# Kernel tuning notes

Measured on AMD Instinct MI355X. Metric: run time of the kernel, lower is better.

The kernel has to match this reference:

```python
import jax, jax.numpy as jnp
import numpy as np

N, D = 1024, 256  # number of matrices (power of 2), matrix dim
EPS = 0.002       # near-identity noise scale to keep 1024-long product stable


def setup_inputs() -> dict:
    key = jax.random.key(0)
    k1, k2 = jax.random.split(key)
    x = jax.random.normal(k1, (1, D), dtype=jnp.float32)
    m = jnp.eye(D, dtype=jnp.float32)[None] + EPS * jax.random.normal(
        k2, (N, D, D), dtype=jnp.float32)
    return {"x": x, "m": m}


def reference(x, m):
    # The torch module performs a Blelloch up-sweep (pairwise bmm) building
    # per-level products, then a down-sweep producing the exclusive prefix
    # applications of x: res[k] = x @ (m_0 @ ... @ m_{k-1}) for k = 0..N.
    # lax.associative_scan with matmul is the idiomatic log-depth tree scan
    # computing the same math: P[k] = m_0 @ ... @ m_k (inclusive, in order).
    P = jax.lax.associative_scan(jnp.matmul, m)      # [N, D, D]
    applied = jnp.matmul(x, P)[:, 0, :]              # [N, D]: x @ P[k]
    # res[0] = x (empty prefix), res[1..N] = x @ P[0..N-1]
    res = jnp.concatenate([x, applied], axis=0)      # [N+1, D]
    return res
```

## Files before the change

### kernel.cpp

```cpp
#include <hip/hip_runtime.h>
#include <hip/hip_bf16.h>


#define D 256
#define DD 65536

typedef __attribute__((ext_vector_type(8))) short short8;
typedef __attribute__((ext_vector_type(4))) float f4;

__device__ __forceinline__ float bf2f(unsigned short u) {
  return __uint_as_float(((unsigned)u) << 16);
}
__device__ __forceinline__ unsigned short f2bf(float f) {
  __hip_bfloat16 h = __float2bfloat16(f);
  unsigned short u;
  __builtin_memcpy(&u, &h, 2);
  return u;
}
__device__ __forceinline__ unsigned f2bf2(float lo, float hi) {
  __hip_bfloat162 h = __float22bfloat162_rn(make_float2(lo, hi));
  unsigned u;
  __builtin_memcpy(&u, &h, 4);
  return u;
}
#define LSWZ(i15, lq) (((((i15) & 15)) + ((lq) << 4)) ^ (lq))

__global__ __launch_bounds__(256, 4) void gemm_mfma(
    const float* __restrict__ aF, const unsigned short* __restrict__ aBf,
    long aMul, long aOff,
    const float* __restrict__ bF, const unsigned short* __restrict__ bBf,
    long bMul, long bOff,
    unsigned short* __restrict__ out)
{
  __shared__ __attribute__((aligned(16))) unsigned short Bs[16384];

  const int  bx  = blockIdx.x;
  const int  nmb = ((int)gridDim.x) >> 4;
  const int  xcd = bx & 7, q = bx >> 3;
  const long mat = (long)(xcd * (nmb >> 3)) + (q >> 4);
  const int  tile = q & 15;
  const int  m0 = (tile >> 2) << 6, n0 = (tile & 3) << 6;
  const long aBase = (mat * aMul + aOff) * (long)DD;
  const long bBase = (mat * bMul + bOff) * (long)DD;
  const int t = threadIdx.x;
  const int w = t >> 6, l = t & 63, lm = l & 15, lq4 = l >> 4;
  const int lswz = l ^ lq4;

  const int R = m0 + (w << 4) + lm;
  short8 areg[8];
  if (aF) {
    const float* ap = aF + aBase + (long)R * D + (lq4 << 3);
#pragma unroll
    for (int kt = 0; kt < 8; ++kt) {
      float4 v0 = *(const float4*)(ap + (kt << 5));
      float4 v1 = *(const float4*)(ap + (kt << 5) + 4);
      if ((R >> 3) == (kt << 2) + lq4) {
        const int j = R & 7;
        if      (j == 0) v0.x -= 1.f;
        else if (j == 1) v0.y -= 1.f;
        else if (j == 2) v0.z -= 1.f;
        else if (j == 3) v0.w -= 1.f;
        else if (j == 4) v1.x -= 1.f;
        else if (j == 5) v1.y -= 1.f;
        else if (j == 6) v1.z -= 1.f;
        else             v1.w -= 1.f;
      }
      union { short8 v8; unsigned u[4]; } ou;
      ou.u[0] = f2bf2(v0.x, v0.y);
      ou.u[1] = f2bf2(v0.z, v0.w);
      ou.u[2] = f2bf2(v1.x, v1.y);
      ou.u[3] = f2bf2(v1.z, v1.w);
      areg[kt] = ou.v8;
    }
  } else {
    const unsigned short* ap = aBf + aBase + (long)R * D + (lq4 << 3);
#pragma unroll
    for (int kt = 0; kt < 8; ++kt)
      areg[kt] = *(const short8*)(ap + (kt << 5));
  }

  {
    const int n4 = (t & 15) << 2;
    const int kb0 = (t >> 4) << 3;
    const int gn = n0 + n4;
#pragma unroll
    for (int kp = 0; kp < 2; ++kp) {
      const int k8 = kb0 + (kp << 7);
      const int lq = (k8 >> 3) & 3, kt = k8 >> 5;
      if (bF) {
        unsigned tmpu[4][4];
        const int rel = gn - k8;
#pragma unroll
        for (int h = 0; h < 2; ++h) {
          float4 va[2], vb[2];
#pragma unroll
          for (int p2 = 0; p2 < 2; ++p2) {
            va[p2] = *(const float4*)(bF + bBase + (long)(k8 + 4 * h + 2 * p2) * D + gn);
            vb[p2] = *(const float4*)(bF + bBase + (long)(k8 + 4 * h + 2 * p2 + 1) * D + gn);
          }
          if (rel == 4 * h) {
            va[0].x -= 1.f; vb[0].y -= 1.f; va[1].z -= 1.f; vb[1].w -= 1.f;
          }
          tmpu[0][2 * h + 0] = f2bf2(va[0].x, vb[0].x);
          tmpu[0][2 * h + 1] = f2bf2(va[1].x, vb[1].x);
          tmpu[1][2 * h + 0] = f2bf2(va[0].y, vb[0].y);
          tmpu[1][2 * h + 1] = f2bf2(va[1].y, vb[1].y);
          tmpu[2][2 * h + 0] = f2bf2(va[0].z, vb[0].z);
          tmpu[2][2 * h + 1] = f2bf2(va[1].z, vb[1].z);
          tmpu[3][2 * h + 0] = f2bf2(va[0].w, vb[0].w);
          tmpu[3][2 * h + 1] = f2bf2(va[1].w, vb[1].w);
        }
#pragma unroll
        for (int jj = 0; jj < 4; ++jj) {
          const int n = n4 + jj;
          const int slot = (((n >> 4) << 3) + kt) * 64 + LSWZ(n, lq);
          uint4 st = { tmpu[jj][0], tmpu[jj][1], tmpu[jj][2], tmpu[jj][3] };
          *(uint4*)&Bs[slot << 3] = st;
        }
      } else {
        __attribute__((aligned(16))) unsigned short tmp[4][8];
#pragma unroll
        for (int kk = 0; kk < 8; ++kk) {
          const ushort4 v = *(const ushort4*)(bBf + bBase + (long)(k8 + kk) * D + gn);
          tmp[0][kk] = v.x; tmp[1][kk] = v.y; tmp[2][kk] = v.z; tmp[3][kk] = v.w;
        }
#pragma unroll
        for (int jj = 0; jj < 4; ++jj) {
          const int n = n4 + jj;
          const int slot = (((n >> 4) << 3) + kt) * 64 + LSWZ(n, lq);
          *(uint4*)&Bs[slot << 3] = *(const uint4*)&tmp[jj][0];
        }
      }
    }
  }
  __syncthreads();

  f4 acc[4] = {{0.f,0.f,0.f,0.f},{0.f,0.f,0.f,0.f},
               {0.f,0.f,0.f,0.f},{0.f,0.f,0.f,0.f}};
#pragma unroll
  for (int kt = 0; kt < 8; ++kt) {
#pragma unroll
    for (int f = 0; f < 4; ++f) {
      const short8 b = *(const short8*)&Bs[((((f << 3) + kt) << 6) + lswz) << 3];
      acc[f] = __builtin_amdgcn_mfma_f32_16x16x32_bf16(areg[kt], b, acc[f], 0, 0, 0);
    }
  }

#pragma unroll
  for (int f = 0; f < 4; ++f) {
    const int gj_l = (f << 4) + lm;
    const int gj   = n0 + gj_l;
#pragma unroll
    for (int r = 0; r < 4; ++r) {
      const int gi_l = (w << 4) + (lq4 << 2) + r;
      const int giG  = m0 + gi_l;
      float da;
      if (aF)
        da = aF[aBase + (long)giG * D + gj] - ((giG == gj) ? 1.f : 0.f);
      else
        da = bf2f(aBf[aBase + (long)giG * D + gj]);
      const int lqB  = (giG >> 3) & 3;
      const int slotB = (((gj_l >> 4) << 3) + (giG >> 5)) * 64 + LSWZ(gj_l, lqB);
      const float db = bf2f(Bs[(slotB << 3) + (giG & 7)]);
      acc[f][r] += da + db;
    }
  }
  __syncthreads();

  unsigned short* Cs = Bs;
#pragma unroll
  for (int f = 0; f < 4; ++f)
#pragma unroll
    for (int r = 0; r < 4; ++r)
      Cs[((w << 4) + (lq4 << 2) + r) * 66 + (f << 4) + lm] = f2bf(acc[f][r]);
  __syncthreads();
  {
    const int row = t >> 2, c0g = (t & 3) << 4;
    const unsigned int* Cw = (const unsigned int*)Cs;
    const int wb = row * 33 + ((t & 3) << 3);
    unsigned int wbuf[8];
#pragma unroll
    for (int i = 0; i < 8; ++i) wbuf[i] = Cw[wb + i];
    unsigned short* og = out + mat * (long)DD + (long)(m0 + row) * D + n0 + c0g;
    uint4 o0 = { wbuf[0], wbuf[1], wbuf[2], wbuf[3] };
    uint4 o1 = { wbuf[4], wbuf[5], wbuf[6], wbuf[7] };
    *(uint4*)og = o0;
    *((uint4*)og + 1) = o1;
  }
}

__device__ __forceinline__ void apply_bf16(const unsigned short* __restrict__ Mb,
                                           float* v, float (*ps)[D],
                                           int t, int col, int kq) {
  const unsigned short* M = Mb + (long)(kq * 64) * D + col;
  float acc = 0.f;
#pragma unroll 8
  for (int i = 0; i < 64; ++i)
    acc += v[kq * 64 + i] * bf2f(M[(long)i * D]);
  ps[kq][col] = acc;
  __syncthreads();
  if (t < D) v[t] += ps[0][t] + ps[1][t] + ps[2][t] + ps[3][t];
  __syncthreads();
}

__global__ __launch_bounds__(1024) void tail_fused(
    const float* __restrict__ x,
    const unsigned short* __restrict__ sp128, const unsigned short* __restrict__ sp64,
    const unsigned short* __restrict__ sp32,  const unsigned short* __restrict__ sp16,
    const unsigned short* __restrict__ sp8,   const unsigned short* __restrict__ sp4,
    const float* __restrict__ m, float* __restrict__ out)
{
  __shared__ float v[D];
  __shared__ float ps[4][D];
  const int c = blockIdx.x, t = threadIdx.x, col = t & 255, kq = t >> 8;
  if (t < D) v[t] = x[t];
  __syncthreads();
  const int L = c << 2;

  int pos = 0;
#pragma unroll 1
  while (pos + 128 <= L) { apply_bf16(sp128 + (long)(pos >> 7) * DD, v, ps, t, col, kq); pos += 128; }
  if (pos + 64 <= L) { apply_bf16(sp64 + (long)(pos >> 6) * DD, v, ps, t, col, kq); pos += 64; }
  if (pos + 32 <= L) { apply_bf16(sp32 + (long)(pos >> 5) * DD, v, ps, t, col, kq); pos += 32; }
  if (pos + 16 <= L) { apply_bf16(sp16 + (long)(pos >> 4) * DD, v, ps, t, col, kq); pos += 16; }
  if (pos + 8 <= L)  { apply_bf16(sp8  + (long)(pos >> 3) * DD, v, ps, t, col, kq); pos += 8; }
  if (pos + 4 <= L)  { apply_bf16(sp4  + (long)(pos >> 2) * DD, v, ps, t, col, kq); pos += 4; }

  if (t < D) out[(long)L * D + t] = v[t];
  const int steps = (c == 255) ? 4 : 3;
#pragma unroll 1
  for (int s = 0; s < steps; ++s) {
    const float* M = m + (long)(L + s) * DD + (long)(kq * 64) * D + col;
    float acc = 0.f;
#pragma unroll 8
    for (int i = 0; i < 64; ++i)
      acc += v[kq * 64 + i] * M[(long)i * D];
    ps[kq][col] = acc;
    __syncthreads();
    if (t < D) {
      const float s2 = ps[0][t] + ps[1][t] + ps[2][t] + ps[3][t];
      v[t] = s2;
      out[(long)(L + s + 1) * D + t] = s2;
    }
    __syncthreads();
  }
}

__global__ __launch_bounds__(256) void fallback_seq(
    const float* __restrict__ x, const float* __restrict__ m,
    float* __restrict__ out)
{
  __shared__ float v[D];
  const int t = threadIdx.x;
  v[t] = x[t];
  __syncthreads();
  for (int k = 0; k < 1024; ++k) {
    out[(long)k * D + t] = v[t];
    const float* M = m + (long)k * DD;
    float acc = 0.f;
    for (int i = 0; i < D; ++i) acc += v[i] * M[(long)i * D + t];
    __syncthreads();
    v[t] = acc;
    __syncthreads();
  }
  out[(long)1024 * D + t] = v[t];
}

extern "C" void kernel_launch(void* const* d_in, const int* in_sizes, int n_in,
                              void* d_out, int out_size, void* d_ws, size_t ws_size,
                              hipStream_t stream) {
  const float* x = (const float*)d_in[0];
  const float* m = (const float*)d_in[1];
  float* out = (float*)d_out;

  char* w8 = (char*)d_ws;
  const size_t MB = 1048576;
  const dim3 blk(256), vblk(1024);

  if (ws_size >= 127 * MB) {
    unsigned short* T2   = (unsigned short*)(w8);
    unsigned short* Qb   = (unsigned short*)(w8 + 64 * MB);
    unsigned short* Q2   = (unsigned short*)(w8 + 96 * MB);
    unsigned short* Q4   = (unsigned short*)(w8 + 112 * MB);
    unsigned short* Rm   = (unsigned short*)(w8 + 120 * MB);
    unsigned short* S64  = (unsigned short*)(w8 + 124 * MB);
    unsigned short* S128 = (unsigned short*)(w8 + 126 * MB);
    gemm_mfma<<<dim3(8192), blk, 0, stream>>>(m, nullptr, 2, 0, m, nullptr, 2, 1, T2);
    gemm_mfma<<<dim3(4096), blk, 0, stream>>>(nullptr, T2, 2, 0, nullptr, T2, 2, 1, Qb);
    gemm_mfma<<<dim3(2048), blk, 0, stream>>>(nullptr, Qb, 2, 0, nullptr, Qb, 2, 1, Q2);
    gemm_mfma<<<dim3(1024), blk, 0, stream>>>(nullptr, Q2, 2, 0, nullptr, Q2, 2, 1, Q4);
    gemm_mfma<<<dim3(512),  blk, 0, stream>>>(nullptr, Q4, 2, 0, nullptr, Q4, 2, 1, Rm);
    gemm_mfma<<<dim3(256),  blk, 0, stream>>>(nullptr, Rm, 2, 0, nullptr, Rm, 2, 1, S64);
    gemm_mfma<<<dim3(128),  blk, 0, stream>>>(nullptr, S64, 2, 0, nullptr, S64, 2, 1, S128);
    tail_fused<<<dim3(256), vblk, 0, stream>>>(x, S128, S64, Rm, Q4, Q2, Qb, m, out);
  } else if (ws_size >= 67108864) {
    unsigned short* buf0 = (unsigned short*)(w8);
    unsigned short* Qb   = (unsigned short*)(w8 + 33554432);
    unsigned short* Q2   = (unsigned short*)(w8);
    unsigned short* Q4   = (unsigned short*)(w8 + 16777216);
    unsigned short* Rm   = (unsigned short*)(w8 + 25165824);
    unsigned short* S64  = (unsigned short*)(w8 + 29360128);
    unsigned short* S128 = (unsigned short*)(w8 + 31457280);
    gemm_mfma<<<dim3(4096), blk, 0, stream>>>(m, nullptr, 2, 0, m, nullptr, 2, 1, buf0);
    gemm_mfma<<<dim3(2048), blk, 0, stream>>>(nullptr, buf0, 2, 0, nullptr, buf0, 2, 1, Qb);
    gemm_mfma<<<dim3(4096), blk, 0, stream>>>(m + 512L * DD, nullptr, 2, 0,
                                              m + 512L * DD, nullptr, 2, 1, buf0);
    gemm_mfma<<<dim3(2048), blk, 0, stream>>>(nullptr, buf0, 2, 0, nullptr, buf0, 2, 1,
                                              Qb + 128L * DD);
    gemm_mfma<<<dim3(2048), blk, 0, stream>>>(nullptr, Qb, 2, 0, nullptr, Qb, 2, 1, Q2);
    gemm_mfma<<<dim3(1024), blk, 0, stream>>>(nullptr, Q2, 2, 0, nullptr, Q2, 2, 1, Q4);
    gemm_mfma<<<dim3(512),  blk, 0, stream>>>(nullptr, Q4, 2, 0, nullptr, Q4, 2, 1, Rm);
    gemm_mfma<<<dim3(256),  blk, 0, stream>>>(nullptr, Rm, 2, 0, nullptr, Rm, 2, 1, S64);
    gemm_mfma<<<dim3(128),  blk, 0, stream>>>(nullptr, S64, 2, 0, nullptr, S64, 2, 1, S128);
    tail_fused<<<dim3(256), vblk, 0, stream>>>(x, S128, S64, Rm, Q4, Q2, Qb, m, out);
  } else {
    fallback_seq<<<dim3(1), blk, 0, stream>>>(x, m, out);
  }
}
```

Measured before the change: 569.1 us.

## Switch pairwise GEMM to 128x128 tiles with K-looped LDS staging

Reworks the pairwise matrix-product kernel so each block computes a 128x128 output tile instead of 64x64, staging both A and B through LDS in 64-wide K steps. Each wave now computes a 4x4 grid of MFMA fragments, which raises operand reuse and cuts the number of blocks by four. The epilogue writes bf16 directly to global memory instead of going through an LDS transpose, and the residual terms are reloaded from global. The risks are fewer blocks for the small late levels (as few as 32), uncoalesced 2-byte stores, and more accumulator registers with the occupancy hint dropped.

```diff
diff --git a/kernel.cpp b/kernel.cpp
--- a/kernel.cpp
+++ b/kernel.cpp
@@ -24,79 +24,88 @@
   return u;
 }
 #define LSWZ(i15, lq) (((((i15) & 15)) + ((lq) << 4)) ^ (lq))
-
-__global__ __launch_bounds__(256, 4) void gemm_mfma(
+#define PSLOT(r, k8) (((((r) >> 4) << 1) + ((k8) >> 5)) * 64 + LSWZ((r), ((k8) >> 3) & 3))
+
+__global__ __launch_bounds__(256) void gemm_mfma(
     const float* __restrict__ aF, const unsigned short* __restrict__ aBf,
     long aMul, long aOff,
     const float* __restrict__ bF, const unsigned short* __restrict__ bBf,
     long bMul, long bOff,
     unsigned short* __restrict__ out)
 {
-  __shared__ __attribute__((aligned(16))) unsigned short Bs[16384];
+  __shared__ __attribute__((aligned(16))) unsigned short As[8192];
+  __shared__ __attribute__((aligned(16))) unsigned short Bs[8192];
 
   const int  bx  = blockIdx.x;
-  const int  nmb = ((int)gridDim.x) >> 4;
+  const int  nmb = ((int)gridDim.x) >> 2;
   const int  xcd = bx & 7, q = bx >> 3;
-  const long mat = (long)(xcd * (nmb >> 3)) + (q >> 4);
-  const int  tile = q & 15;
-  const int  m0 = (tile >> 2) << 6, n0 = (tile & 3) << 6;
+  const long mat = (long)(xcd * (nmb >> 3)) + (q >> 2);
+  const int  tile = q & 3;
+  const int  m0 = (tile >> 1) << 7, n0 = (tile & 1) << 7;
   const long aBase = (mat * aMul + aOff) * (long)DD;
   const long bBase = (mat * bMul + bOff) * (long)DD;
   const int t = threadIdx.x;
   const int w = t >> 6, l = t & 63, lm = l & 15, lq4 = l >> 4;
   const int lswz = l ^ lq4;
-
-  const int R = m0 + (w << 4) + lm;
-  short8 areg[8];
-  if (aF) {
-    const float* ap = aF + aBase + (long)R * D + (lq4 << 3);
-#pragma unroll
-    for (int kt = 0; kt < 8; ++kt) {
-      float4 v0 = *(const float4*)(ap + (kt << 5));
-      float4 v1 = *(const float4*)(ap + (kt << 5) + 4);
-      if ((R >> 3) == (kt << 2) + lq4) {
-        const int j = R & 7;
-        if      (j == 0) v0.x -= 1.f;
-        else if (j == 1) v0.y -= 1.f;
-        else if (j == 2) v0.z -= 1.f;
-        else if (j == 3) v0.w -= 1.f;
-        else if (j == 4) v1.x -= 1.f;
-        else if (j == 5) v1.y -= 1.f;
-        else if (j == 6) v1.z -= 1.f;
-        else             v1.w -= 1.f;
-      }
-      union { short8 v8; unsigned u[4]; } ou;
-      ou.u[0] = f2bf2(v0.x, v0.y);
-      ou.u[1] = f2bf2(v0.z, v0.w);
-      ou.u[2] = f2bf2(v1.x, v1.y);
-      ou.u[3] = f2bf2(v1.z, v1.w);
-      areg[kt] = ou.v8;
-    }
-  } else {
-    const unsigned short* ap = aBf + aBase + (long)R * D + (lq4 << 3);
-#pragma unroll
-    for (int kt = 0; kt < 8; ++kt)
-      areg[kt] = *(const short8*)(ap + (kt << 5));
-  }
-
-  {
-    const int n4 = (t & 15) << 2;
-    const int kb0 = (t >> 4) << 3;
-    const int gn = n0 + n4;
-#pragma unroll
-    for (int kp = 0; kp < 2; ++kp) {
-      const int k8 = kb0 + (kp << 7);
-      const int lq = (k8 >> 3) & 3, kt = k8 >> 5;
+  const int wr = w >> 1, wc = w & 1;
+
+  f4 acc[4][4];
+#pragma unroll
+  for (int i = 0; i < 4; ++i)
+#pragma unroll
+    for (int f = 0; f < 4; ++f)
+      acc[i][f] = (f4){0.f, 0.f, 0.f, 0.f};
+
+  for (int step = 0; step < 4; ++step) {
+    const int kb = step << 6;
+    if (aF) {
+#pragma unroll
+      for (int p = 0; p < 4; ++p) {
+        const int cell = t + (p << 8);
+        const int row = cell >> 3, k8 = (cell & 7) << 3;
+        const int rg = m0 + row, kg = kb + k8;
+        const float* ap = aF + aBase + (long)rg * D + kg;
+        float4 v0 = *(const float4*)ap;
+        float4 v1 = *(const float4*)(ap + 4);
+        const int dj = rg - kg;
+        if (((unsigned)dj) < 8u) {
+          if      (dj == 0) v0.x -= 1.f;
+          else if (dj == 1) v0.y -= 1.f;
+          else if (dj == 2) v0.z -= 1.f;
+          else if (dj == 3) v0.w -= 1.f;
+          else if (dj == 4) v1.x -= 1.f;
+          else if (dj == 5) v1.y -= 1.f;
+          else if (dj == 6) v1.z -= 1.f;
+          else              v1.w -= 1.f;
+        }
+        union { short8 v8; unsigned u[4]; } ou;
+        ou.u[0] = f2bf2(v0.x, v0.y); ou.u[1] = f2bf2(v0.z, v0.w);
+        ou.u[2] = f2bf2(v1.x, v1.y); ou.u[3] = f2bf2(v1.z, v1.w);
+        *(short8*)&As[PSLOT(row, k8) << 3] = ou.v8;
+      }
+    } else {
+#pragma unroll
+      for (int p = 0; p < 4; ++p) {
+        const int cell = t + (p << 8);
+        const int row = cell >> 3, k8 = (cell & 7) << 3;
+        const short8 v = *(const short8*)(aBf + aBase + (long)(m0 + row) * D + kb + k8);
+        *(short8*)&As[PSLOT(row, k8) << 3] = v;
+      }
+    }
+    {
+      const int n4 = (t & 31) << 2;
+      const int k8 = (t >> 5) << 3;
+      const int gn = n0 + n4, kg = kb + k8;
       if (bF) {
         unsigned tmpu[4][4];
-        const int rel = gn - k8;
+        const int rel = gn - kg;
 #pragma unroll
         for (int h = 0; h < 2; ++h) {
           float4 va[2], vb[2];
 #pragma unroll
           for (int p2 = 0; p2 < 2; ++p2) {
-            va[p2] = *(const float4*)(bF + bBase + (long)(k8 + 4 * h + 2 * p2) * D + gn);
-            vb[p2] = *(const float4*)(bF + bBase + (long)(k8 + 4 * h + 2 * p2 + 1) * D + gn);
+            va[p2] = *(const float4*)(bF + bBase + (long)(kg + 4 * h + 2 * p2) * D + gn);
+            vb[p2] = *(const float4*)(bF + bBase + (long)(kg + 4 * h + 2 * p2 + 1) * D + gn);
           }
           if (rel == 4 * h) {
             va[0].x -= 1.f; vb[0].y -= 1.f; va[1].z -= 1.f; vb[1].w -= 1.f;
@@ -113,79 +122,59 @@
 #pragma unroll
         for (int jj = 0; jj < 4; ++jj) {
           const int n = n4 + jj;
-          const int slot = (((n >> 4) << 3) + kt) * 64 + LSWZ(n, lq);
           uint4 st = { tmpu[jj][0], tmpu[jj][1], tmpu[jj][2], tmpu[jj][3] };
-          *(uint4*)&Bs[slot << 3] = st;
+          *(uint4*)&Bs[PSLOT(n, k8) << 3] = st;
         }
       } else {
         __attribute__((aligned(16))) unsigned short tmp[4][8];
 #pragma unroll
         for (int kk = 0; kk < 8; ++kk) {
-          const ushort4 v = *(const ushort4*)(bBf + bBase + (long)(k8 + kk) * D + gn);
+          const ushort4 v = *(const ushort4*)(bBf + bBase + (long)(kg + kk) * D + gn);
           tmp[0][kk] = v.x; tmp[1][kk] = v.y; tmp[2][kk] = v.z; tmp[3][kk] = v.w;
         }
 #pragma unroll
         for (int jj = 0; jj < 4; ++jj) {
           const int n = n4 + jj;
-          const int slot = (((n >> 4) << 3) + kt) * 64 + LSWZ(n, lq);
-          *(uint4*)&Bs[slot << 3] = *(const uint4*)&tmp[jj][0];
-        }
-      }
-    }
-  }
-  __syncthreads();
-
-  f4 acc[4] = {{0.f,0.f,0.f,0.f},{0.f,0.f,0.f,0.f},
-               {0.f,0.f,0.f,0.f},{0.f,0.f,0.f,0.f}};
-#pragma unroll
-  for (int kt = 0; kt < 8; ++kt) {
-#pragma unroll
-    for (int f = 0; f < 4; ++f) {
-      const short8 b = *(const short8*)&Bs[((((f << 3) + kt) << 6) + lswz) << 3];
-      acc[f] = __builtin_amdgcn_mfma_f32_16x16x32_bf16(areg[kt], b, acc[f], 0, 0, 0);
-    }
-  }
-
-#pragma unroll
-  for (int f = 0; f < 4; ++f) {
-    const int gj_l = (f << 4) + lm;
-    const int gj   = n0 + gj_l;
+          *(uint4*)&Bs[PSLOT(n, k8) << 3] = *(const uint4*)&tmp[jj][0];
+        }
+      }
+    }
+    __syncthreads();
+#pragma unroll
+    for (int kt = 0; kt < 2; ++kt) {
+      short8 a_[4];
+#pragma unroll
+      for (int i = 0; i < 4; ++i)
+        a_[i] = *(const short8*)&As[(((((wr << 2) + i) << 1) + kt) * 64 + lswz) << 3];
+#pragma unroll
+      for (int f = 0; f < 4; ++f) {
+        const short8 b = *(const short8*)&Bs[(((((wc << 2) + f) << 1) + kt) * 64 + lswz) << 3];
+#pragma unroll
+        for (int i = 0; i < 4; ++i)
+          acc[i][f] = __builtin_amdgcn_mfma_f32_16x16x32_bf16(a_[i], b, acc[i][f], 0, 0, 0);
+      }
+    }
+    __syncthreads();
+  }
+
+#pragma unroll
+  for (int i = 0; i < 4; ++i) {
 #pragma unroll
     for (int r = 0; r < 4; ++r) {
-      const int gi_l = (w << 4) + (lq4 << 2) + r;
-      const int giG  = m0 + gi_l;
-      float da;
-      if (aF)
-        da = aF[aBase + (long)giG * D + gj] - ((giG == gj) ? 1.f : 0.f);
-      else
-        da = bf2f(aBf[aBase + (long)giG * D + gj]);
-      const int lqB  = (giG >> 3) & 3;
-      const int slotB = (((gj_l >> 4) << 3) + (giG >> 5)) * 64 + LSWZ(gj_l, lqB);
-      const float db = bf2f(Bs[(slotB << 3) + (giG & 7)]);
-      acc[f][r] += da + db;
-    }
-  }
-  __syncthreads();
-
-  unsigned short* Cs = Bs;
-#pragma unroll
-  for (int f = 0; f < 4; ++f)
-#pragma unroll
-    for (int r = 0; r < 4; ++r)
-      Cs[((w << 4) + (lq4 << 2) + r) * 66 + (f << 4) + lm] = f2bf(acc[f][r]);
-  __syncthreads();
-  {
-    const int row = t >> 2, c0g = (t & 3) << 4;
-    const unsigned int* Cw = (const unsigned int*)Cs;
-    const int wb = row * 33 + ((t & 3) << 3);
-    unsigned int wbuf[8];
-#pragma unroll
-    for (int i = 0; i < 8; ++i) wbuf[i] = Cw[wb + i];
-    unsigned short* og = out + mat * (long)DD + (long)(m0 + row) * D + n0 + c0g;
-    uint4 o0 = { wbuf[0], wbuf[1], wbuf[2], wbuf[3] };
-    uint4 o1 = { wbuf[4], wbuf[5], wbuf[6], wbuf[7] };
-    *(uint4*)og = o0;
-    *((uint4*)og + 1) = o1;
+      const int rowg = m0 + (wr << 6) + (i << 4) + (lq4 << 2) + r;
+      const long rA = aBase + (long)rowg * D;
+      const long rB = bBase + (long)rowg * D;
+      const long rO = mat * (long)DD + (long)rowg * D;
+#pragma unroll
+      for (int f = 0; f < 4; ++f) {
+        const int colg = n0 + (wc << 6) + (f << 4) + lm;
+        const float da = aF ? (aF[rA + colg] - ((rowg == colg) ? 1.f : 0.f))
+                            : bf2f(aBf[rA + colg]);
+        const float db = bF ? (bF[rB + colg] - ((rowg == colg) ? 1.f : 0.f))
+                            : bf2f(bBf[rB + colg]);
+        out[rO + colg] = f2bf(acc[i][f][r] + da + db);
+      }
+    }
   }
 }
 
@@ -285,13 +274,13 @@
     unsigned short* Rm   = (unsigned short*)(w8 + 120 * MB);
     unsigned short* S64  = (unsigned short*)(w8 + 124 * MB);
     unsigned short* S128 = (unsigned short*)(w8 + 126 * MB);
-    gemm_mfma<<<dim3(8192), blk, 0, stream>>>(m, nullptr, 2, 0, m, nullptr, 2, 1, T2);
-    gemm_mfma<<<dim3(4096), blk, 0, stream>>>(nullptr, T2, 2, 0, nullptr, T2, 2, 1, Qb);
-    gemm_mfma<<<dim3(2048), blk, 0, stream>>>(nullptr, Qb, 2, 0, nullptr, Qb, 2, 1, Q2);
-    gemm_mfma<<<dim3(1024), blk, 0, stream>>>(nullptr, Q2, 2, 0, nullptr, Q2, 2, 1, Q4);
-    gemm_mfma<<<dim3(512),  blk, 0, stream>>>(nullptr, Q4, 2, 0, nullptr, Q4, 2, 1, Rm);
-    gemm_mfma<<<dim3(256),  blk, 0, stream>>>(nullptr, Rm, 2, 0, nullptr, Rm, 2, 1, S64);
-    gemm_mfma<<<dim3(128),  blk, 0, stream>>>(nullptr, S64, 2, 0, nullptr, S64, 2, 1, S128);
+    gemm_mfma<<<dim3(2048), blk, 0, stream>>>(m, nullptr, 2, 0, m, nullptr, 2, 1, T2);
+    gemm_mfma<<<dim3(1024), blk, 0, stream>>>(nullptr, T2, 2, 0, nullptr, T2, 2, 1, Qb);
+    gemm_mfma<<<dim3(512),  blk, 0, stream>>>(nullptr, Qb, 2, 0, nullptr, Qb, 2, 1, Q2);
+    gemm_mfma<<<dim3(256),  blk, 0, stream>>>(nullptr, Q2, 2, 0, nullptr, Q2, 2, 1, Q4);
+    gemm_mfma<<<dim3(128),  blk, 0, stream>>>(nullptr, Q4, 2, 0, nullptr, Q4, 2, 1, Rm);
+    gemm_mfma<<<dim3(64),   blk, 0, stream>>>(nullptr, Rm, 2, 0, nullptr, Rm, 2, 1, S64);
+    gemm_mfma<<<dim3(32),   blk, 0, stream>>>(nullptr, S64, 2, 0, nullptr, S64, 2, 1, S128);
     tail_fused<<<dim3(256), vblk, 0, stream>>>(x, S128, S64, Rm, Q4, Q2, Qb, m, out);
   } else if (ws_size >= 67108864) {
     unsigned short* buf0 = (unsigned short*)(w8);
@@ -301,17 +290,17 @@
     unsigned short* Rm   = (unsigned short*)(w8 + 25165824);
     unsigned short* S64  = (unsigned short*)(w8 + 29360128);
     unsigned short* S128 = (unsigned short*)(w8 + 31457280);
-    gemm_mfma<<<dim3(4096), blk, 0, stream>>>(m, nullptr, 2, 0, m, nullptr, 2, 1, buf0);
-    gemm_mfma<<<dim3(2048), blk, 0, stream>>>(nullptr, buf0, 2, 0, nullptr, buf0, 2, 1, Qb);
-    gemm_mfma<<<dim3(4096), blk, 0, stream>>>(m + 512L * DD, nullptr, 2, 0,
+    gemm_mfma<<<dim3(1024), blk, 0, stream>>>(m, nullptr, 2, 0, m, nullptr, 2, 1, buf0);
+    gemm_mfma<<<dim3(512),  blk, 0, stream>>>(nullptr, buf0, 2, 0, nullptr, buf0, 2, 1, Qb);
+    gemm_mfma<<<dim3(1024), blk, 0, stream>>>(m + 512L * DD, nullptr, 2, 0,
                                               m + 512L * DD, nullptr, 2, 1, buf0);
-    gemm_mfma<<<dim3(2048), blk, 0, stream>>>(nullptr, buf0, 2, 0, nullptr, buf0, 2, 1,
+    gemm_mfma<<<dim3(512),  blk, 0, stream>>>(nullptr, buf0, 2, 0, nullptr, buf0, 2, 1,
                                               Qb + 128L * DD);
-    gemm_mfma<<<dim3(2048), blk, 0, stream>>>(nullptr, Qb, 2, 0, nullptr, Qb, 2, 1, Q2);
-    gemm_mfma<<<dim3(1024), blk, 0, stream>>>(nullptr, Q2, 2, 0, nullptr, Q2, 2, 1, Q4);
-    gemm_mfma<<<dim3(512),  blk, 0, stream>>>(nullptr, Q4, 2, 0, nullptr, Q4, 2, 1, Rm);
-    gemm_mfma<<<dim3(256),  blk, 0, stream>>>(nullptr, Rm, 2, 0, nullptr, Rm, 2, 1, S64);
-    gemm_mfma<<<dim3(128),  blk, 0, stream>>>(nullptr, S64, 2, 0, nullptr, S64, 2, 1, S128);
+    gemm_mfma<<<dim3(512),  blk, 0, stream>>>(nullptr, Qb, 2, 0, nullptr, Qb, 2, 1, Q2);
+    gemm_mfma<<<dim3(256),  blk, 0, stream>>>(nullptr, Q2, 2, 0, nullptr, Q2, 2, 1, Q4);
+    gemm_mfma<<<dim3(128),  blk, 0, stream>>>(nullptr, Q4, 2, 0, nullptr, Q4, 2, 1, Rm);
+    gemm_mfma<<<dim3(64),   blk, 0, stream>>>(nullptr, Rm, 2, 0, nullptr, Rm, 2, 1, S64);
+    gemm_mfma<<<dim3(32),   blk, 0, stream>>>(nullptr, S64, 2, 0, nullptr, S64, 2, 1, S128);
     tail_fused<<<dim3(256), vblk, 0, stream>>>(x, S128, S64, Rm, Q4, Q2, Qb, m, out);
   } else {
     fallback_seq<<<dim3(1), blk, 0, stream>>>(x, m, out);
```

Result: slower. 754.0 us (+32.5%).

## Fuse up-sweep GEMM levels into one cooperative kernel and vectorize tail matvec

Applied to the files above, without the earlier changes.

Replaces seven separate per-level GEMM launches with one persistent cooperative kernel of 1024 blocks. It loops over tree levels with grid-wide syncs between them, which removes launch gaps and tail effects of the shrinking late levels. The tail matvec now gives each thread four columns with 16-row chunks and vector loads, reduced across 16 partial rows in shared memory. Risks: the cooperative launch needs all 1024 blocks co-resident, and grid.sync costs extra; the code falls back to the old launches if the cooperative launch fails.

```diff
diff --git a/kernel.cpp b/kernel.cpp
--- a/kernel.cpp
+++ b/kernel.cpp
@@ -1,5 +1,8 @@
 #include <hip/hip_runtime.h>
 #include <hip/hip_bf16.h>
+#include <hip/hip_cooperative_groups.h>
+
+namespace cg = cooperative_groups;
 
 
 #define D 256
@@ -25,18 +28,17 @@
 }
 #define LSWZ(i15, lq) (((((i15) & 15)) + ((lq) << 4)) ^ (lq))
 
-__global__ __launch_bounds__(256, 4) void gemm_mfma(
+__device__ __forceinline__ void do_tile(
     const float* __restrict__ aF, const unsigned short* __restrict__ aBf,
     long aMul, long aOff,
     const float* __restrict__ bF, const unsigned short* __restrict__ bBf,
     long bMul, long bOff,
-    unsigned short* __restrict__ out)
+    unsigned short* __restrict__ out, int job, int njobs)
 {
   __shared__ __attribute__((aligned(16))) unsigned short Bs[16384];
 
-  const int  bx  = blockIdx.x;
-  const int  nmb = ((int)gridDim.x) >> 4;
-  const int  xcd = bx & 7, q = bx >> 3;
+  const int  nmb = njobs >> 4;
+  const int  xcd = job & 7, q = job >> 3;
   const long mat = (long)(xcd * (nmb >> 3)) + (q >> 4);
   const int  tile = q & 15;
   const int  m0 = (tile >> 2) << 6, n0 = (tile & 3) << 6;
@@ -187,19 +189,60 @@
     *(uint4*)og = o0;
     *((uint4*)og + 1) = o1;
   }
+  __syncthreads();
+}
+
+__global__ __launch_bounds__(256, 4) void gemm_mfma(
+    const float* __restrict__ aF, const unsigned short* __restrict__ aBf,
+    long aMul, long aOff,
+    const float* __restrict__ bF, const unsigned short* __restrict__ bBf,
+    long bMul, long bOff,
+    unsigned short* __restrict__ out)
+{
+  do_tile(aF, aBf, aMul, aOff, bF, bBf, bMul, bOff, out, blockIdx.x, gridDim.x);
+}
+
+__global__ __launch_bounds__(256, 4) void tree_coop(
+    const float* __restrict__ m,
+    unsigned short* __restrict__ T2,  unsigned short* __restrict__ Qb,
+    unsigned short* __restrict__ Q2,  unsigned short* __restrict__ Q4,
+    unsigned short* __restrict__ Rm,  unsigned short* __restrict__ S64,
+    unsigned short* __restrict__ S128)
+{
+  cg::grid_group grid = cg::this_grid();
+  unsigned short* outs[7] = {T2, Qb, Q2, Q4, Rm, S64, S128};
+#pragma unroll 1
+  for (int lev = 0; lev < 7; ++lev) {
+    const int njobs = 8192 >> lev;
+    const float* aF = (lev == 0) ? m : nullptr;
+    const unsigned short* aB = (lev == 0) ? nullptr : outs[lev - 1];
+#pragma unroll 1
+    for (int job = blockIdx.x; job < njobs; job += gridDim.x)
+      do_tile(aF, aB, 2, 0, aF, aB, 2, 1, outs[lev], job, njobs);
+    grid.sync();
+  }
 }
 
 __device__ __forceinline__ void apply_bf16(const unsigned short* __restrict__ Mb,
                                            float* v, float (*ps)[D],
-                                           int t, int col, int kq) {
-  const unsigned short* M = Mb + (long)(kq * 64) * D + col;
-  float acc = 0.f;
-#pragma unroll 8
-  for (int i = 0; i < 64; ++i)
-    acc += v[kq * 64 + i] * bf2f(M[(long)i * D]);
-  ps[kq][col] = acc;
-  __syncthreads();
-  if (t < D) v[t] += ps[0][t] + ps[1][t] + ps[2][t] + ps[3][t];
+                                           int t, int col4, int q) {
+  const unsigned short* Mp = Mb + (long)(q * 16) * D + col4;
+  float a0 = 0.f, a1 = 0.f, a2 = 0.f, a3 = 0.f;
+#pragma unroll
+  for (int i = 0; i < 16; ++i) {
+    const ushort4 u = *(const ushort4*)(Mp + (long)i * D);
+    const float vi = v[q * 16 + i];
+    a0 += vi * bf2f(u.x); a1 += vi * bf2f(u.y);
+    a2 += vi * bf2f(u.z); a3 += vi * bf2f(u.w);
+  }
+  *(float4*)&ps[q][col4] = make_float4(a0, a1, a2, a3);
+  __syncthreads();
+  if (t < D) {
+    float s = 0.f;
+#pragma unroll
+    for (int j = 0; j < 16; ++j) s += ps[j][t];
+    v[t] += s;
+  }
   __syncthreads();
 }
 
@@ -211,34 +254,40 @@
     const float* __restrict__ m, float* __restrict__ out)
 {
   __shared__ float v[D];
-  __shared__ float ps[4][D];
-  const int c = blockIdx.x, t = threadIdx.x, col = t & 255, kq = t >> 8;
+  __shared__ float ps[16][D];
+  const int c = blockIdx.x, t = threadIdx.x;
+  const int col4 = (t & 63) << 2, q = t >> 6;
   if (t < D) v[t] = x[t];
   __syncthreads();
   const int L = c << 2;
 
   int pos = 0;
 #pragma unroll 1
-  while (pos + 128 <= L) { apply_bf16(sp128 + (long)(pos >> 7) * DD, v, ps, t, col, kq); pos += 128; }
-  if (pos + 64 <= L) { apply_bf16(sp64 + (long)(pos >> 6) * DD, v, ps, t, col, kq); pos += 64; }
-  if (pos + 32 <= L) { apply_bf16(sp32 + (long)(pos >> 5) * DD, v, ps, t, col, kq); pos += 32; }
-  if (pos + 16 <= L) { apply_bf16(sp16 + (long)(pos >> 4) * DD, v, ps, t, col, kq); pos += 16; }
-  if (pos + 8 <= L)  { apply_bf16(sp8  + (long)(pos >> 3) * DD, v, ps, t, col, kq); pos += 8; }
-  if (pos + 4 <= L)  { apply_bf16(sp4  + (long)(pos >> 2) * DD, v, ps, t, col, kq); pos += 4; }
+  while (pos + 128 <= L) { apply_bf16(sp128 + (long)(pos >> 7) * DD, v, ps, t, col4, q); pos += 128; }
+  if (pos + 64 <= L) { apply_bf16(sp64 + (long)(pos >> 6) * DD, v, ps, t, col4, q); pos += 64; }
+  if (pos + 32 <= L) { apply_bf16(sp32 + (long)(pos >> 5) * DD, v, ps, t, col4, q); pos += 32; }
+  if (pos + 16 <= L) { apply_bf16(sp16 + (long)(pos >> 4) * DD, v, ps, t, col4, q); pos += 16; }
+  if (pos + 8 <= L)  { apply_bf16(sp8  + (long)(pos >> 3) * DD, v, ps, t, col4, q); pos += 8; }
+  if (pos + 4 <= L)  { apply_bf16(sp4  + (long)(pos >> 2) * DD, v, ps, t, col4, q); pos += 4; }
 
   if (t < D) out[(long)L * D + t] = v[t];
   const int steps = (c == 255) ? 4 : 3;
 #pragma unroll 1
   for (int s = 0; s < steps; ++s) {
-    const float* M = m + (long)(L + s) * DD + (long)(kq * 64) * D + col;
-    float acc = 0.f;
-#pragma unroll 8
-    for (int i = 0; i < 64; ++i)
-      acc += v[kq * 64 + i] * M[(long)i * D];
-    ps[kq][col] = acc;
+    const float* Mp = m + (long)(L + s) * DD + (long)(q * 16) * D + col4;
+    float a0 = 0.f, a1 = 0.f, a2 = 0.f, a3 = 0.f;
+#pragma unroll
+    for (int i = 0; i < 16; ++i) {
+      const float4 u = *(const float4*)(Mp + (long)i * D);
+      const float vi = v[q * 16 + i];
+      a0 += vi * u.x; a1 += vi * u.y; a2 += vi * u.z; a3 += vi * u.w;
+    }
+    *(float4*)&ps[q][col4] = make_float4(a0, a1, a2, a3);
     __syncthreads();
     if (t < D) {
-      const float s2 = ps[0][t] + ps[1][t] + ps[2][t] + ps[3][t];
+      float s2 = 0.f;
+#pragma unroll
+      for (int j = 0; j < 16; ++j) s2 += ps[j][t];
       v[t] = s2;
       out[(long)(L + s + 1) * D + t] = s2;
     }
@@ -285,13 +334,20 @@
     unsigned short* Rm   = (unsigned short*)(w8 + 120 * MB);
     unsigned short* S64  = (unsigned short*)(w8 + 124 * MB);
     unsigned short* S128 = (unsigned short*)(w8 + 126 * MB);
-    gemm_mfma<<<dim3(8192), blk, 0, stream>>>(m, nullptr, 2, 0, m, nullptr, 2, 1, T2);
-    gemm_mfma<<<dim3(4096), blk, 0, stream>>>(nullptr, T2, 2, 0, nullptr, T2, 2, 1, Qb);
-    gemm_mfma<<<dim3(2048), blk, 0, stream>>>(nullptr, Qb, 2, 0, nullptr, Qb, 2, 1, Q2);
-    gemm_mfma<<<dim3(1024), blk, 0, stream>>>(nullptr, Q2, 2, 0, nullptr, Q2, 2, 1, Q4);
-    gemm_mfma<<<dim3(512),  blk, 0, stream>>>(nullptr, Q4, 2, 0, nullptr, Q4, 2, 1, Rm);
-    gemm_mfma<<<dim3(256),  blk, 0, stream>>>(nullptr, Rm, 2, 0, nullptr, Rm, 2, 1, S64);
-    gemm_mfma<<<dim3(128),  blk, 0, stream>>>(nullptr, S64, 2, 0, nullptr, S64, 2, 1, S128);
+    const float* mm = m;
+    void* args[] = { (void*)&mm, (void*)&T2, (void*)&Qb, (void*)&Q2,
+                     (void*)&Q4, (void*)&Rm, (void*)&S64, (void*)&S128 };
+    hipError_t e = hipLaunchCooperativeKernel((const void*)tree_coop,
+                                              dim3(1024), blk, args, 0, stream);
+    if (e != hipSuccess) {
+      gemm_mfma<<<dim3(8192), blk, 0, stream>>>(m, nullptr, 2, 0, m, nullptr, 2, 1, T2);
+      gemm_mfma<<<dim3(4096), blk, 0, stream>>>(nullptr, T2, 2, 0, nullptr, T2, 2, 1, Qb);
+      gemm_mfma<<<dim3(2048), blk, 0, stream>>>(nullptr, Qb, 2, 0, nullptr, Qb, 2, 1, Q2);
+      gemm_mfma<<<dim3(1024), blk, 0, stream>>>(nullptr, Q2, 2, 0, nullptr, Q2, 2, 1, Q4);
+      gemm_mfma<<<dim3(512),  blk, 0, stream>>>(nullptr, Q4, 2, 0, nullptr, Q4, 2, 1, Rm);
+      gemm_mfma<<<dim3(256),  blk, 0, stream>>>(nullptr, Rm, 2, 0, nullptr, Rm, 2, 1, S64);
+      gemm_mfma<<<dim3(128),  blk, 0, stream>>>(nullptr, S64, 2, 0, nullptr, S64, 2, 1, S128);
+    }
     tail_fused<<<dim3(256), vblk, 0, stream>>>(x, S128, S64, Rm, Q4, Q2, Qb, m, out);
   } else if (ws_size >= 67108864) {
     unsigned short* buf0 = (unsigned short*)(w8);
```

Result: slower. 1.462 ms (+156.9%).
